# Performance work log

Measured on AMD Instinct MI355X. Metric: run time of the kernel, lower is better.

## Reference

```python
import jax, jax.numpy as jnp
import numpy as np

D_MODEL = 1024
NUM_HEADS = 16
HEAD_DIM = D_MODEL // NUM_HEADS
ROPE_THETA = 10000.0


def apply_rope(x):
    # x: (B, H, S, d_k) interleaved-pair RoPE, angles pos / theta^(2i/d_k)
    S, d_k = x.shape[-2], x.shape[-1]
    inv_freq = ROPE_THETA ** (jnp.arange(0, d_k, 2, dtype=jnp.float32) / d_k)
    ang = jnp.arange(S, dtype=jnp.float32)[:, None] / inv_freq[None, :]  # (S, d_k/2)
    cos, sin = jnp.cos(ang), jnp.sin(ang)
    xp = x.reshape(x.shape[:-1] + (d_k // 2, 2))
    x0, x1 = xp[..., 0], xp[..., 1]
    out = jnp.stack([x0 * cos - x1 * sin, x0 * sin + x1 * cos], axis=-1)
    return out.reshape(x.shape)


def setup_inputs() -> dict:
    key = jax.random.key(0)
    k1, k2, k3 = jax.random.split(key, 3)
    B, S = 2, 2048
    std = 2.0 / (D_MODEL + 3 * D_MODEL)
    std_o = 2.0 / (D_MODEL + D_MODEL)
    return {
        "x": jax.random.normal(k1, (B, S, D_MODEL), dtype=jnp.float32),
        "W_qkv": jax.random.normal(k2, (3 * D_MODEL, D_MODEL), dtype=jnp.float32) * std,
        "W_o": jax.random.normal(k3, (D_MODEL, D_MODEL), dtype=jnp.float32) * std_o,
    }


def reference(x, W_qkv, W_o):
    B, S, d_model = x.shape
    H, d_k = NUM_HEADS, HEAD_DIM
    qkv = jnp.einsum('bsi,oi->bso', x, W_qkv)  # (B, S, 3*d_model)
    Q, K, V = jnp.split(qkv, 3, axis=-1)
    # (B, S, d_model) -> (B, H, S, d_k)
    def to_heads(t):
        return t.reshape(B, S, H, d_k).transpose(0, 2, 1, 3)
    Q, K, V = to_heads(Q), to_heads(K), to_heads(V)
    Q, K = apply_rope(Q), apply_rope(K)
    scores = jnp.einsum('bhqd,bhkd->bhqk', Q, K) / jnp.sqrt(jnp.float32(d_k))
    causal = jnp.tril(jnp.ones((S, S), dtype=bool))
    scores = jnp.where(causal, scores, -jnp.inf)
    attn = jax.nn.softmax(scores, axis=-1)
    out = jnp.einsum('bhqk,bhkd->bhqd', attn, V)
    out = out.transpose(0, 2, 1, 3).reshape(B, S, d_model)
    return jnp.einsum('bsi,oi->bso', out, W_o)
```

## Files before the change

kernel.cpp:

```cpp
#include <hip/hip_runtime.h>
#include <math.h>

#define kB 2
#define kS 2048
#define kD 1024
#define kH 16
#define kDk 64
#define kM (kB * kS)
#define kLog2Theta 13.287712379549449
#define C_SCALE 0.18033688011112042f

typedef __attribute__((ext_vector_type(4))) float f32x4;
typedef __attribute__((ext_vector_type(16))) float f32x16;
typedef __attribute__((ext_vector_type(8))) __bf16 bf16x8;

__device__ __forceinline__ ushort f2bf(float f) {
  uint u = __float_as_uint(f);
  return (ushort)((u + 0x7fffu + ((u >> 16) & 1u)) >> 16);
}
__device__ __forceinline__ uint cvt_pk_bf16(float lo, float hi) {
  uint r;
  asm("v_cvt_pk_bf16_f32 %0, %1, %2" : "=v"(r) : "v"(lo), "v"(hi));
  return r;
}

typedef __attribute__((address_space(1))) void gvoid;
typedef __attribute__((address_space(3))) void lvoid;
__device__ __forceinline__ void load_lds16(const void* g, void* l) {
  __builtin_amdgcn_global_load_lds((gvoid*)g, (lvoid*)l, 16, 0, 0);
}

__global__ __launch_bounds__(256) void rope_table_kernel(float2* __restrict__ tab) {
  const int i = blockIdx.x * 256 + threadIdx.x;
  const int s = i >> 5, p = i & 31;
  const double ang = (double)s * exp2(-(double)p * (kLog2Theta / 32.0));
  tab[i] = make_float2((float)cos(ang), (float)sin(ang));
}

__global__ __launch_bounds__(256) void cast_all_kernel(
    const float* __restrict__ x, const float* __restrict__ wq,
    const float* __restrict__ wo, ushort* __restrict__ xb,
    ushort* __restrict__ wqb, ushort* __restrict__ wob) {
  const int i = blockIdx.x * 256 + threadIdx.x;
  const float* src;
  ushort* dst;
  int off;
  if (i < 1048576) {
    src = x; dst = xb; off = i;
  } else if (i < 1048576 + 786432) {
    src = wq; dst = wqb; off = i - 1048576;
  } else {
    src = wo; dst = wob; off = i - 1835008;
  }
  const float4 v = reinterpret_cast<const float4*>(src)[off];
  ushort4 o;
  o.x = f2bf(v.x); o.y = f2bf(v.y); o.z = f2bf(v.z); o.w = f2bf(v.w);
  reinterpret_cast<ushort4*>(dst)[off] = o;
}

__global__ __launch_bounds__(256) void vtrans_kernel(
    const ushort* __restrict__ v, ushort* __restrict__ vt) {
  __shared__ ushort T[64 * 66];
  const int bh = blockIdx.y, st = blockIdx.x;
  const int tid = threadIdx.x;
  const ushort* vp = v + ((size_t)bh * kS + st * 64) * kDk;
#pragma unroll
  for (int u = 0; u < 2; ++u) {
    const int idx = u * 256 + tid;
    const int r = idx >> 3, c = (idx & 7) << 3;
    const uint4 d4 = *reinterpret_cast<const uint4*>(&vp[r * 64 + c]);
    uint* dst = reinterpret_cast<uint*>(&T[r * 66 + c]);
    dst[0] = d4.x; dst[1] = d4.y; dst[2] = d4.z; dst[3] = d4.w;
  }
  __syncthreads();
  const int d = tid >> 2, seg = tid & 3;
  ushort tmp[16];
#pragma unroll
  for (int j = 0; j < 16; ++j) tmp[j] = T[(seg * 16 + j) * 66 + d];
  ushort* dst = vt + ((size_t)bh * kDk + d) * kS + st * 64 + seg * 16;
  *reinterpret_cast<uint4*>(dst) = *reinterpret_cast<uint4*>(tmp);
  *reinterpret_cast<uint4*>(dst + 8) = *reinterpret_cast<uint4*>(tmp + 8);
}

__device__ __forceinline__ void gemm_mainloop(
    const ushort* __restrict__ A, const ushort* __restrict__ B,
    int m0, int n0, int tid, ushort* As, ushort* Bs, f32x4 acc[4][4]) {
  const int lane = tid & 63;
  const int wid = tid >> 6;
  const int wm = (wid >> 1) << 6, wn = (wid & 1) << 6;
  const int fr = lane & 15, fq = lane >> 4;

  for (int k0 = 0; k0 < kD; k0 += 64) {
#pragma unroll
    for (int u = 0; u < 4; ++u) {
      const int c = u * 256 + tid;
      const int r = c >> 3, kc = (c & 7) << 3;
      load_lds16(&A[(size_t)(m0 + r) * kD + k0 + kc], &As[c << 3]);
      load_lds16(&B[(size_t)(n0 + r) * kD + k0 + kc], &Bs[c << 3]);
    }
    __syncthreads();
#pragma unroll
    for (int kk = 0; kk < 64; kk += 32) {
      bf16x8 af[4], bfr[4];
#pragma unroll
      for (int f = 0; f < 4; ++f) {
        af[f]  = *reinterpret_cast<const bf16x8*>(&As[(wm + f * 16 + fr) * 64 + kk + fq * 8]);
        bfr[f] = *reinterpret_cast<const bf16x8*>(&Bs[(wn + f * 16 + fr) * 64 + kk + fq * 8]);
      }
#pragma unroll
      for (int i = 0; i < 4; ++i)
#pragma unroll
        for (int j = 0; j < 4; ++j)
          acc[i][j] = __builtin_amdgcn_mfma_f32_16x16x32_bf16(af[i], bfr[j], acc[i][j], 0, 0, 0);
    }
    __syncthreads();
  }
}

__global__ __launch_bounds__(256) void qkv_mfma_kernel(
    const ushort* __restrict__ xb, const ushort* __restrict__ wqb,
    const float2* __restrict__ tab,
    ushort* __restrict__ q, ushort* __restrict__ k, ushort* __restrict__ v) {
  __shared__ ushort As[128 * 64];
  __shared__ ushort Bs[128 * 64];
  const int tid = threadIdx.x;
  const int m0 = blockIdx.y << 7, n0 = blockIdx.x << 7;
  f32x4 acc[4][4];
#pragma unroll
  for (int i = 0; i < 4; ++i)
#pragma unroll
    for (int j = 0; j < 4; ++j) acc[i][j] = {0.f, 0.f, 0.f, 0.f};

  gemm_mainloop(xb, wqb, m0, n0, tid, As, Bs, acc);

  const int lane = tid & 63;
  const int wid = tid >> 6;
  const int wm = (wid >> 1) << 6, wn = (wid & 1) << 6;
  const int fr = lane & 15, fq = lane >> 4;
  const int t = n0 >> 10;
  ushort* dst = (t == 0) ? q : (t == 1) ? k : v;

#pragma unroll
  for (int i = 0; i < 4; ++i) {
    const int mbase = m0 + wm + i * 16 + fq * 4;
#pragma unroll
    for (int j = 0; j < 4; ++j) {
      const int n = n0 + wn + j * 16 + fr;
      const int h = (n >> 6) & 15, d = n & 63;
#pragma unroll
      for (int r = 0; r < 4; ++r) {
        const int m = mbase + r;
        const int b = m >> 11, s = m & (kS - 1);
        float val = acc[i][j][r];
        if (t < 2) {
          const float2 cs = tab[(s << 5) + (d >> 1)];
          const float partner = __shfl_xor(val, 1);
          val = (d & 1) ? (partner * cs.y + val * cs.x)
                        : (val * cs.x - partner * cs.y);
        }
        if (t == 0) val *= C_SCALE;
        dst[(((size_t)((b << 4) + h) << 11) + s) * kDk + d] = f2bf(val);
      }
    }
  }
}

__global__ __launch_bounds__(256) void proj_mfma_kernel(
    const ushort* __restrict__ ab, const ushort* __restrict__ wob,
    float* __restrict__ out) {
  __shared__ ushort As[128 * 64];
  __shared__ ushort Bs[128 * 64];
  const int tid = threadIdx.x;
  const int m0 = blockIdx.y << 7, n0 = blockIdx.x << 7;
  f32x4 acc[4][4];
#pragma unroll
  for (int i = 0; i < 4; ++i)
#pragma unroll
    for (int j = 0; j < 4; ++j) acc[i][j] = {0.f, 0.f, 0.f, 0.f};

  gemm_mainloop(ab, wob, m0, n0, tid, As, Bs, acc);

  const int lane = tid & 63;
  const int wid = tid >> 6;
  const int wm = (wid >> 1) << 6, wn = (wid & 1) << 6;
  const int fr = lane & 15, fq = lane >> 4;
#pragma unroll
  for (int i = 0; i < 4; ++i)
#pragma unroll
    for (int j = 0; j < 4; ++j)
#pragma unroll
      for (int r = 0; r < 4; ++r)
        out[(size_t)(m0 + wm + i * 16 + fq * 4 + r) * kD + n0 + wn + j * 16 + fr] =
            acc[i][j][r];
}

__global__ __launch_bounds__(256) void attn_mfma_kernel(
    const ushort* __restrict__ q, const ushort* __restrict__ k,
    const ushort* __restrict__ vt, ushort* __restrict__ ob) {
  __shared__ ushort smem[32768];
  const int tid = threadIdx.x;
  const int lane = tid & 63;
  const int wq = tid >> 6;
  const int l5 = lane >> 5;
  const int ln = lane & 31;
  const int swz = (ln & 7) << 4;

  const int idx = blockIdx.x;
  const int grp = idx >> 5, bh = idx & 31;
  const int qi = (grp < 8) ? (15 - grp) : (grp - 8);
  const int qb = qi << 7;
  const int nt = qi + 1;

  const ushort* qp = q + (size_t)bh * kS * kDk;
  const ushort* kp = k + (size_t)bh * kS * kDk;
  const ushort* vp = vt + (size_t)bh * kDk * kS;

  bf16x8 bq[4];
#pragma unroll
  for (int kk = 0; kk < 4; ++kk)
    bq[kk] = *reinterpret_cast<const bf16x8*>(
        &qp[(size_t)(qb + wq * 32 + ln) * kDk + kk * 16 + l5 * 8]);

  f32x16 acc_o[2];
#pragma unroll
  for (int db = 0; db < 2; ++db)
#pragma unroll
    for (int r = 0; r < 16; ++r) acc_o[db][r] = 0.f;
  float l_run = 0.f;

  auto stage = [&](int kt, int buf) {
    ushort* Kd = smem + buf * 16384;
    ushort* Vd = Kd + 8192;
#pragma unroll
    for (int u = 0; u < 4; ++u) {
      const int c = u * 256 + tid;
      {
        const int r = c >> 3, sl = c & 7;
        load_lds16(&kp[(size_t)(kt * 128 + r) * kDk + ((sl ^ (r & 7)) << 3)],
                   &Kd[c << 3]);
      }
      {
        const int r = c >> 4, sl = c & 15;
        load_lds16(&vp[(size_t)r * kS + kt * 128 + ((sl ^ (r & 7)) << 3)],
                   &Vd[c << 3]);
      }
    }
  };

  stage(0, 0);

  for (int kt = 0; kt < nt; ++kt) {
    const int cur = kt & 1;
    __syncthreads();
    if (kt + 1 < nt) stage(kt + 1, cur ^ 1);

    const char* KsB = reinterpret_cast<const char*>(smem + cur * 16384);
    const char* VtsB = KsB + 16384;

    f32x16 accs[4];
    __builtin_amdgcn_s_setprio(1);
#pragma unroll
    for (int cb = 0; cb < 4; ++cb) {
#pragma unroll
      for (int r = 0; r < 16; ++r) accs[cb][r] = 0.f;
#pragma unroll
      for (int kk = 0; kk < 4; ++kk) {
        const bf16x8 av = *reinterpret_cast<const bf16x8*>(
            KsB + (cb * 32 + ln) * 128 + ((kk * 32 + l5 * 16) ^ swz));
        accs[cb] = __builtin_amdgcn_mfma_f32_32x32x16_bf16(av, bq[kk], accs[cb], 0, 0, 0);
      }
    }
    __builtin_amdgcn_s_setprio(0);

    if (kt == qi) {
      const int lim = (wq << 5) + ln;
#pragma unroll
      for (int cb = 0; cb < 4; ++cb)
#pragma unroll
        for (int r = 0; r < 16; ++r) {
          const int key = cb * 32 + (r & 3) + 8 * (r >> 2) + 4 * l5;
          if (key > lim) accs[cb][r] = -INFINITY;
        }
    }

    uint c8[4][8];
    float lsum = 0.f;
#pragma unroll
    for (int cb = 0; cb < 4; ++cb) {
      float s0 = 0.f, s1 = 0.f, s2 = 0.f, s3 = 0.f;
      float p[16];
#pragma unroll
      for (int r = 0; r < 16; ++r) {
        p[r] = exp2f(accs[cb][r]);
        if ((r & 3) == 0) s0 += p[r];
        else if ((r & 3) == 1) s1 += p[r];
        else if ((r & 3) == 2) s2 += p[r];
        else s3 += p[r];
      }
      lsum += (s0 + s1) + (s2 + s3);
#pragma unroll
      for (int t = 0; t < 8; ++t)
        c8[cb][t] = cvt_pk_bf16(p[2 * t], p[2 * t + 1]);
    }
    l_run += lsum;

    __builtin_amdgcn_s_setprio(1);
#pragma unroll
    for (int kb = 0; kb < 8; ++kb) {
      const int cb = kb >> 1, base = (kb & 1) * 4;
      const uint a0 = c8[cb][base + 0], a1 = c8[cb][base + 1];
      const uint b0 = c8[cb][base + 2], b1 = c8[cb][base + 3];
      const uint sa0 = (uint)__shfl_xor((int)a0, 32);
      const uint sa1 = (uint)__shfl_xor((int)a1, 32);
      const uint sb0 = (uint)__shfl_xor((int)b0, 32);
      const uint sb1 = (uint)__shfl_xor((int)b1, 32);
      uint4 dw;
      dw.x = l5 ? sb0 : a0;
      dw.y = l5 ? sb1 : a1;
      dw.z = l5 ? b0 : sa0;
      dw.w = l5 ? b1 : sa1;
      const bf16x8 pa = *reinterpret_cast<const bf16x8*>(&dw);
#pragma unroll
      for (int db = 0; db < 2; ++db) {
        const bf16x8 av = *reinterpret_cast<const bf16x8*>(
            VtsB + (db * 32 + ln) * 256 + ((kb * 32 + l5 * 16) ^ swz));
        acc_o[db] = __builtin_amdgcn_mfma_f32_32x32x16_bf16(av, pa, acc_o[db], 0, 0, 0);
      }
    }
    __builtin_amdgcn_s_setprio(0);
  }

  const float l_tot = l_run + __shfl_xor(l_run, 32);
  const float linv = 1.f / l_tot;

  __syncthreads();
  char* OsB = reinterpret_cast<char*>(smem);
  const int orow = wq * 32 + ln;
#pragma unroll
  for (int db = 0; db < 2; ++db)
#pragma unroll
    for (int t = 0; t < 8; ++t) {
      const int reg = 2 * t;
      const int d = db * 32 + (reg & 3) + 8 * (reg >> 2) + 4 * l5;
      const uint pk2 = cvt_pk_bf16(acc_o[db][reg] * linv, acc_o[db][reg + 1] * linv);
      *reinterpret_cast<uint*>(OsB + orow * 128 + ((d * 2) ^ swz)) = pk2;
    }
  __syncthreads();
  const int b = bh >> 4, h = bh & 15;
  const int qrw = tid >> 1, half = tid & 1;
  ushort* orow_g = ob + ((size_t)(b * kS + qb + qrw)) * kD + h * kDk + half * 32;
#pragma unroll
  for (int sl = 0; sl < 4; ++sl) {
    const uint4 vdat = *reinterpret_cast<const uint4*>(
        OsB + qrw * 128 + ((half * 64 + sl * 16) ^ ((qrw & 7) << 4)));
    *reinterpret_cast<uint4*>(orow_g + sl * 8) = vdat;
  }
}

extern "C" void kernel_launch(void* const* d_in, const int* in_sizes, int n_in,
                              void* d_out, int out_size, void* d_ws,
                              size_t ws_size, hipStream_t stream) {
  const float* x = (const float*)d_in[0];
  const float* wqkv = (const float*)d_in[1];
  const float* wo = (const float*)d_in[2];
  float* out = (float*)d_out;
  char* w = (char*)d_ws;
  const size_t MB = 1024 * 1024;
  ushort* qb  = (ushort*)(w + 0 * MB);
  ushort* kb  = (ushort*)(w + 8 * MB);
  ushort* vb  = (ushort*)(w + 16 * MB);
  ushort* xb  = (ushort*)(w + 24 * MB);
  ushort* wqb = (ushort*)(w + 32 * MB);
  ushort* wob = (ushort*)(w + 38 * MB);
  float2* tab = (float2*)(w + 40 * MB);
  ushort* vtb = (ushort*)(w + 41 * MB);
  ushort* attnb = xb;

  hipLaunchKernelGGL(rope_table_kernel, dim3(256), dim3(256), 0, stream, tab);
  hipLaunchKernelGGL(cast_all_kernel, dim3(8192), dim3(256), 0, stream,
                     x, wqkv, wo, xb, wqb, wob);
  hipLaunchKernelGGL(qkv_mfma_kernel, dim3(3 * kD / 128, kM / 128), dim3(256),
                     0, stream, xb, wqb, tab, qb, kb, vb);
  hipLaunchKernelGGL(vtrans_kernel, dim3(kS / 64, kB * kH), dim3(256), 0,
                     stream, vb, vtb);
  hipLaunchKernelGGL(attn_mfma_kernel, dim3(512), dim3(256), 0, stream,
                     qb, kb, vtb, attnb);
  hipLaunchKernelGGL(proj_mfma_kernel, dim3(kD / 128, kM / 128), dim3(256), 0,
                     stream, attnb, wob, out);
}
```

Before: 163.2 us.

## Use 256x256 double-buffered swizzled LDS GEMM tiles for QKV and output projections

```diff
diff --git a/kernel.cpp b/kernel.cpp
--- a/kernel.cpp
+++ b/kernel.cpp
@@ -7,6 +7,7 @@
 #define kH 16
 #define kDk 64
 #define kM (kB * kS)
+#define kNT (kD / 64)
 #define kLog2Theta 13.287712379549449
 #define C_SCALE 0.18033688011112042f
 
@@ -82,70 +83,107 @@
   *reinterpret_cast<uint4*>(dst + 8) = *reinterpret_cast<uint4*>(tmp + 8);
 }
 
-__device__ __forceinline__ void gemm_mainloop(
+__device__ __forceinline__ void gemm256_mainloop(
     const ushort* __restrict__ A, const ushort* __restrict__ B,
-    int m0, int n0, int tid, ushort* As, ushort* Bs, f32x4 acc[4][4]) {
+    int m0, int n0, int tid,
+    ushort* As0, ushort* Bs0, ushort* As1, ushort* Bs1,
+    f32x4 (&acc)[8][4]) {
   const int lane = tid & 63;
-  const int wid = tid >> 6;
-  const int wm = (wid >> 1) << 6, wn = (wid & 1) << 6;
+  const int wmi = (tid >> 6) >> 2;
+  const int wni = (tid >> 6) & 3;
   const int fr = lane & 15, fq = lane >> 4;
 
-  for (int k0 = 0; k0 < kD; k0 += 64) {
-#pragma unroll
-    for (int u = 0; u < 4; ++u) {
-      const int c = u * 256 + tid;
-      const int r = c >> 3, kc = (c & 7) << 3;
-      load_lds16(&A[(size_t)(m0 + r) * kD + k0 + kc], &As[c << 3]);
-      load_lds16(&B[(size_t)(n0 + r) * kD + k0 + kc], &Bs[c << 3]);
-    }
-    __syncthreads();
-#pragma unroll
-    for (int kk = 0; kk < 64; kk += 32) {
-      bf16x8 af[4], bfr[4];
-#pragma unroll
-      for (int f = 0; f < 4; ++f) {
-        af[f]  = *reinterpret_cast<const bf16x8*>(&As[(wm + f * 16 + fr) * 64 + kk + fq * 8]);
-        bfr[f] = *reinterpret_cast<const bf16x8*>(&Bs[(wn + f * 16 + fr) * 64 + kk + fq * 8]);
-      }
-#pragma unroll
-      for (int i = 0; i < 4; ++i)
-#pragma unroll
-        for (int j = 0; j < 4; ++j)
-          acc[i][j] = __builtin_amdgcn_mfma_f32_16x16x32_bf16(af[i], bfr[j], acc[i][j], 0, 0, 0);
-    }
-    __syncthreads();
-  }
-}
-
-__global__ __launch_bounds__(256) void qkv_mfma_kernel(
+  auto stage_tile = [&](int k0, ushort* Ad, ushort* Bd) {
+#pragma unroll
+    for (int half = 0; half < 2; ++half)
+#pragma unroll
+      for (int u = 0; u < 2; ++u) {
+        const int c = u * 512 + tid;
+        const int r = c >> 3, sl = c & 7;
+        const int gcol = k0 + ((sl ^ (r & 7)) << 3);
+        const int loff = ((half * 128 + r) << 6) + (sl << 3);
+        load_lds16(&A[(size_t)(m0 + half * 128 + r) * kD + gcol], &Ad[loff]);
+        load_lds16(&B[(size_t)(n0 + half * 128 + r) * kD + gcol], &Bd[loff]);
+      }
+  };
+  auto frag = [&](const ushort* S, int row, int kk) -> bf16x8 {
+    const int off = ((kk << 5) + (fq << 3)) ^ ((fr & 7) << 3);
+    return *reinterpret_cast<const bf16x8*>(&S[(row << 6) + off]);
+  };
+
+  stage_tile(0, As0, Bs0);
+  asm volatile("s_waitcnt vmcnt(0)" ::: "memory");
+  __builtin_amdgcn_s_barrier();
+
+  auto tile = [&](int kt, const ushort* cA, const ushort* cB,
+                  ushort* nA, ushort* nB) {
+#pragma unroll
+    for (int p = 0; p < 4; ++p) {
+      const int iset = (p & 1) << 2, jset = (p >> 1) << 1;
+      bf16x8 af[4][2], bfv[2][2];
+#pragma unroll
+      for (int i2 = 0; i2 < 4; ++i2)
+#pragma unroll
+        for (int kk = 0; kk < 2; ++kk)
+          af[i2][kk] = frag(cA, (wmi << 7) + (iset + i2) * 16 + fr, kk);
+#pragma unroll
+      for (int j2 = 0; j2 < 2; ++j2)
+#pragma unroll
+        for (int kk = 0; kk < 2; ++kk)
+          bfv[j2][kk] = frag(cB, (wni << 6) + (jset + j2) * 16 + fr, kk);
+      if (p == 0 && kt + 1 < kNT) stage_tile((kt + 1) << 6, nA, nB);
+      __builtin_amdgcn_s_barrier();
+      asm volatile("s_waitcnt lgkmcnt(0)" ::: "memory");
+      __builtin_amdgcn_sched_barrier(0);
+      __builtin_amdgcn_s_setprio(1);
+#pragma unroll
+      for (int i2 = 0; i2 < 4; ++i2)
+#pragma unroll
+        for (int j2 = 0; j2 < 2; ++j2)
+#pragma unroll
+          for (int kk = 0; kk < 2; ++kk)
+            acc[iset + i2][jset + j2] = __builtin_amdgcn_mfma_f32_16x16x32_bf16(
+                af[i2][kk], bfv[j2][kk], acc[iset + i2][jset + j2], 0, 0, 0);
+      __builtin_amdgcn_s_setprio(0);
+      if (p == 3) asm volatile("s_waitcnt vmcnt(0)" ::: "memory");
+      __builtin_amdgcn_s_barrier();
+    }
+  };
+
+  for (int kt = 0; kt < kNT; kt += 2) {
+    tile(kt, As0, Bs0, As1, Bs1);
+    tile(kt + 1, As1, Bs1, As0, Bs0);
+  }
+}
+
+__global__ __launch_bounds__(512, 2) void qkv_mfma_kernel(
     const ushort* __restrict__ xb, const ushort* __restrict__ wqb,
     const float2* __restrict__ tab,
     ushort* __restrict__ q, ushort* __restrict__ k, ushort* __restrict__ v) {
-  __shared__ ushort As[128 * 64];
-  __shared__ ushort Bs[128 * 64];
+  __shared__ ushort As0[256 * 64], Bs0[256 * 64];
+  __shared__ ushort As1[256 * 64], Bs1[256 * 64];
   const int tid = threadIdx.x;
-  const int m0 = blockIdx.y << 7, n0 = blockIdx.x << 7;
-  f32x4 acc[4][4];
-#pragma unroll
-  for (int i = 0; i < 4; ++i)
+  const int m0 = blockIdx.y << 8, n0 = blockIdx.x << 8;
+  f32x4 acc[8][4];
+#pragma unroll
+  for (int i = 0; i < 8; ++i)
 #pragma unroll
     for (int j = 0; j < 4; ++j) acc[i][j] = {0.f, 0.f, 0.f, 0.f};
 
-  gemm_mainloop(xb, wqb, m0, n0, tid, As, Bs, acc);
+  gemm256_mainloop(xb, wqb, m0, n0, tid, As0, Bs0, As1, Bs1, acc);
 
   const int lane = tid & 63;
-  const int wid = tid >> 6;
-  const int wm = (wid >> 1) << 6, wn = (wid & 1) << 6;
+  const int wmi = (tid >> 6) >> 2, wni = (tid >> 6) & 3;
   const int fr = lane & 15, fq = lane >> 4;
   const int t = n0 >> 10;
   ushort* dst = (t == 0) ? q : (t == 1) ? k : v;
 
 #pragma unroll
-  for (int i = 0; i < 4; ++i) {
-    const int mbase = m0 + wm + i * 16 + fq * 4;
+  for (int i = 0; i < 8; ++i) {
+    const int mbase = m0 + (wmi << 7) + i * 16 + fq * 4;
 #pragma unroll
     for (int j = 0; j < 4; ++j) {
-      const int n = n0 + wn + j * 16 + fr;
+      const int n = n0 + (wni << 6) + j * 16 + fr;
       const int h = (n >> 6) & 15, d = n & 63;
 #pragma unroll
       for (int r = 0; r < 4; ++r) {
@@ -165,33 +203,32 @@
   }
 }
 
-__global__ __launch_bounds__(256) void proj_mfma_kernel(
+__global__ __launch_bounds__(512, 2) void proj_mfma_kernel(
     const ushort* __restrict__ ab, const ushort* __restrict__ wob,
     float* __restrict__ out) {
-  __shared__ ushort As[128 * 64];
-  __shared__ ushort Bs[128 * 64];
+  __shared__ ushort As0[256 * 64], Bs0[256 * 64];
+  __shared__ ushort As1[256 * 64], Bs1[256 * 64];
   const int tid = threadIdx.x;
-  const int m0 = blockIdx.y << 7, n0 = blockIdx.x << 7;
-  f32x4 acc[4][4];
-#pragma unroll
-  for (int i = 0; i < 4; ++i)
+  const int m0 = blockIdx.y << 8, n0 = blockIdx.x << 8;
+  f32x4 acc[8][4];
+#pragma unroll
+  for (int i = 0; i < 8; ++i)
 #pragma unroll
     for (int j = 0; j < 4; ++j) acc[i][j] = {0.f, 0.f, 0.f, 0.f};
 
-  gemm_mainloop(ab, wob, m0, n0, tid, As, Bs, acc);
+  gemm256_mainloop(ab, wob, m0, n0, tid, As0, Bs0, As1, Bs1, acc);
 
   const int lane = tid & 63;
-  const int wid = tid >> 6;
-  const int wm = (wid >> 1) << 6, wn = (wid & 1) << 6;
+  const int wmi = (tid >> 6) >> 2, wni = (tid >> 6) & 3;
   const int fr = lane & 15, fq = lane >> 4;
 #pragma unroll
-  for (int i = 0; i < 4; ++i)
+  for (int i = 0; i < 8; ++i)
 #pragma unroll
     for (int j = 0; j < 4; ++j)
 #pragma unroll
       for (int r = 0; r < 4; ++r)
-        out[(size_t)(m0 + wm + i * 16 + fq * 4 + r) * kD + n0 + wn + j * 16 + fr] =
-            acc[i][j][r];
+        out[(size_t)(m0 + (wmi << 7) + i * 16 + fq * 4 + r) * kD +
+            n0 + (wni << 6) + j * 16 + fr] = acc[i][j][r];
 }
 
 __global__ __launch_bounds__(256) void attn_mfma_kernel(
@@ -379,12 +416,12 @@
   hipLaunchKernelGGL(rope_table_kernel, dim3(256), dim3(256), 0, stream, tab);
   hipLaunchKernelGGL(cast_all_kernel, dim3(8192), dim3(256), 0, stream,
                      x, wqkv, wo, xb, wqb, wob);
-  hipLaunchKernelGGL(qkv_mfma_kernel, dim3(3 * kD / 128, kM / 128), dim3(256),
+  hipLaunchKernelGGL(qkv_mfma_kernel, dim3(3 * kD / 256, kM / 256), dim3(512),
                      0, stream, xb, wqb, tab, qb, kb, vb);
   hipLaunchKernelGGL(vtrans_kernel, dim3(kS / 64, kB * kH), dim3(256), 0,
                      stream, vb, vtb);
   hipLaunchKernelGGL(attn_mfma_kernel, dim3(512), dim3(256), 0, stream,
                      qb, kb, vtb, attnb);
-  hipLaunchKernelGGL(proj_mfma_kernel, dim3(kD / 128, kM / 128), dim3(256), 0,
+  hipLaunchKernelGGL(proj_mfma_kernel, dim3(kD / 256, kM / 256), dim3(512), 0,
                      stream, attnb, wob, out);
 }
```

Result: slower. 176.8 us, median of 4 (+8.3%).

## Rewrite GEMM mainloop with double-buffered LDS, 32x32 MFMA and larger QKV tiles

Applied to the files above, without the earlier changes.

```diff
diff --git a/kernel.cpp b/kernel.cpp
--- a/kernel.cpp
+++ b/kernel.cpp
@@ -7,6 +7,7 @@
 #define kH 16
 #define kDk 64
 #define kM (kB * kS)
+#define kNT (kD / 64)
 #define kLog2Theta 13.287712379549449
 #define C_SCALE 0.18033688011112042f
 
@@ -82,74 +83,139 @@
   *reinterpret_cast<uint4*>(dst + 8) = *reinterpret_cast<uint4*>(tmp + 8);
 }
 
-__device__ __forceinline__ void gemm_mainloop(
+template <int BM, int BN, int WM, int WN>
+__device__ __forceinline__ void gemm_sub(
     const ushort* __restrict__ A, const ushort* __restrict__ B,
-    int m0, int n0, int tid, ushort* As, ushort* Bs, f32x4 acc[4][4]) {
+    int m0, int n0, int tid,
+    ushort* As0, ushort* Bs0, ushort* As1, ushort* Bs1,
+    f32x16 (&acc)[BM / (WM * 32)][BN / (WN * 32)]) {
+  constexpr int TM = BM / (WM * 32);
+  constexpr int TN = BN / (WN * 32);
+  constexpr int NTHR = WM * WN * 64;
+  constexpr int LGK = TM + TN;
   const int lane = tid & 63;
+  const int ln = lane & 31, l5 = lane >> 5;
   const int wid = tid >> 6;
-  const int wm = (wid >> 1) << 6, wn = (wid & 1) << 6;
-  const int fr = lane & 15, fq = lane >> 4;
-
-  for (int k0 = 0; k0 < kD; k0 += 64) {
-#pragma unroll
-    for (int u = 0; u < 4; ++u) {
-      const int c = u * 256 + tid;
-      const int r = c >> 3, kc = (c & 7) << 3;
-      load_lds16(&A[(size_t)(m0 + r) * kD + k0 + kc], &As[c << 3]);
-      load_lds16(&B[(size_t)(n0 + r) * kD + k0 + kc], &Bs[c << 3]);
-    }
+  const int wmi = wid / WN, wni = wid % WN;
+
+  auto stage_tile = [&](int k0, ushort* Ad, ushort* Bd) {
+#pragma unroll
+    for (int t = 0; t < BM * 8 / NTHR; ++t) {
+      const int c = t * NTHR + tid;
+      const int h = c & 1, r = (c >> 1) & 31, kk = (c >> 6) & 3, rb = c >> 8;
+      load_lds16(&A[(size_t)(m0 + rb * 32 + r) * kD + k0 + kk * 16 + h * 8],
+                 &Ad[c * 8]);
+    }
+#pragma unroll
+    for (int t = 0; t < BN * 8 / NTHR; ++t) {
+      const int c = t * NTHR + tid;
+      const int h = c & 1, r = (c >> 1) & 31, kk = (c >> 6) & 3, rb = c >> 8;
+      load_lds16(&B[(size_t)(n0 + rb * 32 + r) * kD + k0 + kk * 16 + h * 8],
+                 &Bd[c * 8]);
+    }
+  };
+  auto rd = [&](const ushort* S, int blk, int kk) -> bf16x8 {
+    return *reinterpret_cast<const bf16x8*>(
+        &S[((blk * 4 + kk) * 32 + ln) * 16 + l5 * 8]);
+  };
+
+  bf16x8 aX[TM], bX[TN], aY[TM], bY[TN];
+  auto rdX = [&](const ushort* cA, const ushort* cB, int kk) {
+#pragma unroll
+    for (int i = 0; i < TM; ++i) aX[i] = rd(cA, wmi * TM + i, kk);
+#pragma unroll
+    for (int j = 0; j < TN; ++j) bX[j] = rd(cB, wni * TN + j, kk);
+  };
+  auto rdY = [&](const ushort* cA, const ushort* cB, int kk) {
+#pragma unroll
+    for (int i = 0; i < TM; ++i) aY[i] = rd(cA, wmi * TM + i, kk);
+#pragma unroll
+    for (int j = 0; j < TN; ++j) bY[j] = rd(cB, wni * TN + j, kk);
+  };
+  auto mmaX = [&]() {
+    __builtin_amdgcn_s_setprio(1);
+#pragma unroll
+    for (int i = 0; i < TM; ++i)
+#pragma unroll
+      for (int j = 0; j < TN; ++j)
+        acc[i][j] = __builtin_amdgcn_mfma_f32_32x32x16_bf16(
+            aX[i], bX[j], acc[i][j], 0, 0, 0);
+    __builtin_amdgcn_s_setprio(0);
+  };
+  auto mmaY = [&]() {
+    __builtin_amdgcn_s_setprio(1);
+#pragma unroll
+    for (int i = 0; i < TM; ++i)
+#pragma unroll
+      for (int j = 0; j < TN; ++j)
+        acc[i][j] = __builtin_amdgcn_mfma_f32_32x32x16_bf16(
+            aY[i], bY[j], acc[i][j], 0, 0, 0);
+    __builtin_amdgcn_s_setprio(0);
+  };
+
+  stage_tile(0, As0, Bs0);
+  __syncthreads();
+
+  auto tile = [&](const ushort* cA, const ushort* cB, bool pf, int k0n,
+                  ushort* nA, ushort* nB) {
+    rdX(cA, cB, 0);
+    if (pf) stage_tile(k0n, nA, nB);
+    rdY(cA, cB, 1);
+    asm volatile("s_waitcnt lgkmcnt(%0)" ::"n"(LGK) : "memory");
+    __builtin_amdgcn_sched_barrier(0);
+    mmaX();
+    rdX(cA, cB, 2);
+    asm volatile("s_waitcnt lgkmcnt(%0)" ::"n"(LGK) : "memory");
+    __builtin_amdgcn_sched_barrier(0);
+    mmaY();
+    rdY(cA, cB, 3);
+    asm volatile("s_waitcnt lgkmcnt(%0)" ::"n"(LGK) : "memory");
+    __builtin_amdgcn_sched_barrier(0);
+    mmaX();
+    asm volatile("s_waitcnt lgkmcnt(0)" :: : "memory");
+    __builtin_amdgcn_sched_barrier(0);
+    mmaY();
     __syncthreads();
-#pragma unroll
-    for (int kk = 0; kk < 64; kk += 32) {
-      bf16x8 af[4], bfr[4];
-#pragma unroll
-      for (int f = 0; f < 4; ++f) {
-        af[f]  = *reinterpret_cast<const bf16x8*>(&As[(wm + f * 16 + fr) * 64 + kk + fq * 8]);
-        bfr[f] = *reinterpret_cast<const bf16x8*>(&Bs[(wn + f * 16 + fr) * 64 + kk + fq * 8]);
-      }
-#pragma unroll
-      for (int i = 0; i < 4; ++i)
-#pragma unroll
-        for (int j = 0; j < 4; ++j)
-          acc[i][j] = __builtin_amdgcn_mfma_f32_16x16x32_bf16(af[i], bfr[j], acc[i][j], 0, 0, 0);
-    }
-    __syncthreads();
+  };
+
+  for (int kt = 0; kt < kNT; kt += 2) {
+    tile(As0, Bs0, kt + 1 < kNT, (kt + 1) << 6, As1, Bs1);
+    tile(As1, Bs1, kt + 2 < kNT, (kt + 2) << 6, As0, Bs0);
   }
 }
 
-__global__ __launch_bounds__(256) void qkv_mfma_kernel(
+__global__ __launch_bounds__(512) void qkv_mfma_kernel(
     const ushort* __restrict__ xb, const ushort* __restrict__ wqb,
     const float2* __restrict__ tab,
     ushort* __restrict__ q, ushort* __restrict__ k, ushort* __restrict__ v) {
-  __shared__ ushort As[128 * 64];
-  __shared__ ushort Bs[128 * 64];
+  __shared__ ushort As0[256 * 64], Bs0[256 * 64];
+  __shared__ ushort As1[256 * 64], Bs1[256 * 64];
   const int tid = threadIdx.x;
-  const int m0 = blockIdx.y << 7, n0 = blockIdx.x << 7;
-  f32x4 acc[4][4];
+  const int m0 = blockIdx.y << 8, n0 = blockIdx.x << 8;
+  f32x16 acc[4][2];
 #pragma unroll
   for (int i = 0; i < 4; ++i)
 #pragma unroll
-    for (int j = 0; j < 4; ++j) acc[i][j] = {0.f, 0.f, 0.f, 0.f};
-
-  gemm_mainloop(xb, wqb, m0, n0, tid, As, Bs, acc);
-
-  const int lane = tid & 63;
-  const int wid = tid >> 6;
-  const int wm = (wid >> 1) << 6, wn = (wid & 1) << 6;
-  const int fr = lane & 15, fq = lane >> 4;
+    for (int j = 0; j < 2; ++j)
+#pragma unroll
+      for (int r = 0; r < 16; ++r) acc[i][j][r] = 0.f;
+
+  gemm_sub<256, 256, 2, 4>(xb, wqb, m0, n0, tid, As0, Bs0, As1, Bs1, acc);
+
+  const int lane = tid & 63, ln = lane & 31, l5 = lane >> 5;
+  const int wid = tid >> 6, wmi = wid >> 2, wni = wid & 3;
   const int t = n0 >> 10;
   ushort* dst = (t == 0) ? q : (t == 1) ? k : v;
 
 #pragma unroll
-  for (int i = 0; i < 4; ++i) {
-    const int mbase = m0 + wm + i * 16 + fq * 4;
-#pragma unroll
-    for (int j = 0; j < 4; ++j) {
-      const int n = n0 + wn + j * 16 + fr;
+  for (int i = 0; i < 4; ++i)
+#pragma unroll
+    for (int j = 0; j < 2; ++j) {
+      const int n = n0 + (wni * 2 + j) * 32 + ln;
       const int h = (n >> 6) & 15, d = n & 63;
 #pragma unroll
-      for (int r = 0; r < 4; ++r) {
-        const int m = mbase + r;
+      for (int r = 0; r < 16; ++r) {
+        const int m = m0 + (wmi * 4 + i) * 32 + (r & 3) + 8 * (r >> 2) + 4 * l5;
         const int b = m >> 11, s = m & (kS - 1);
         float val = acc[i][j][r];
         if (t < 2) {
@@ -162,36 +228,38 @@
         dst[(((size_t)((b << 4) + h) << 11) + s) * kDk + d] = f2bf(val);
       }
     }
-  }
 }
 
 __global__ __launch_bounds__(256) void proj_mfma_kernel(
     const ushort* __restrict__ ab, const ushort* __restrict__ wob,
     float* __restrict__ out) {
-  __shared__ ushort As[128 * 64];
-  __shared__ ushort Bs[128 * 64];
+  __shared__ ushort As0[128 * 64], Bs0[128 * 64];
+  __shared__ ushort As1[128 * 64], Bs1[128 * 64];
   const int tid = threadIdx.x;
   const int m0 = blockIdx.y << 7, n0 = blockIdx.x << 7;
-  f32x4 acc[4][4];
-#pragma unroll
-  for (int i = 0; i < 4; ++i)
-#pragma unroll
-    for (int j = 0; j < 4; ++j) acc[i][j] = {0.f, 0.f, 0.f, 0.f};
-
-  gemm_mainloop(ab, wob, m0, n0, tid, As, Bs, acc);
-
-  const int lane = tid & 63;
-  const int wid = tid >> 6;
-  const int wm = (wid >> 1) << 6, wn = (wid & 1) << 6;
-  const int fr = lane & 15, fq = lane >> 4;
-#pragma unroll
-  for (int i = 0; i < 4; ++i)
-#pragma unroll
-    for (int j = 0; j < 4; ++j)
-#pragma unroll
-      for (int r = 0; r < 4; ++r)
-        out[(size_t)(m0 + wm + i * 16 + fq * 4 + r) * kD + n0 + wn + j * 16 + fr] =
-            acc[i][j][r];
+  f32x16 acc[2][2];
+#pragma unroll
+  for (int i = 0; i < 2; ++i)
+#pragma unroll
+    for (int j = 0; j < 2; ++j)
+#pragma unroll
+      for (int r = 0; r < 16; ++r) acc[i][j][r] = 0.f;
+
+  gemm_sub<128, 128, 2, 2>(ab, wob, m0, n0, tid, As0, Bs0, As1, Bs1, acc);
+
+  const int lane = tid & 63, ln = lane & 31, l5 = lane >> 5;
+  const int wid = tid >> 6, wmi = wid >> 1, wni = wid & 1;
+#pragma unroll
+  for (int i = 0; i < 2; ++i)
+#pragma unroll
+    for (int j = 0; j < 2; ++j) {
+      const int n = n0 + (wni * 2 + j) * 32 + ln;
+#pragma unroll
+      for (int r = 0; r < 16; ++r) {
+        const int m = m0 + (wmi * 2 + i) * 32 + (r & 3) + 8 * (r >> 2) + 4 * l5;
+        out[(size_t)m * kD + n] = acc[i][j][r];
+      }
+    }
 }
 
 __global__ __launch_bounds__(256) void attn_mfma_kernel(
@@ -379,7 +447,7 @@
   hipLaunchKernelGGL(rope_table_kernel, dim3(256), dim3(256), 0, stream, tab);
   hipLaunchKernelGGL(cast_all_kernel, dim3(8192), dim3(256), 0, stream,
                      x, wqkv, wo, xb, wqb, wob);
-  hipLaunchKernelGGL(qkv_mfma_kernel, dim3(3 * kD / 128, kM / 128), dim3(256),
+  hipLaunchKernelGGL(qkv_mfma_kernel, dim3(3 * kD / 256, kM / 256), dim3(512),
                      0, stream, xb, wqb, tab, qb, kb, vb);
   hipLaunchKernelGGL(vtrans_kernel, dim3(kS / 64, kB * kH), dim3(256), 0,
                      stream, vb, vtb);
```

New measurement: 150.1 us. -8.0%, faster.

## Double-buffer GEMM mainloop with XOR-swizzled LDS and prefetch overlap

Applied to the files above, without the earlier changes.

```diff
diff --git a/kernel.cpp b/kernel.cpp
--- a/kernel.cpp
+++ b/kernel.cpp
@@ -7,6 +7,7 @@
 #define kH 16
 #define kDk 64
 #define kM (kB * kS)
+#define kNT (kD / 64)
 #define kLog2Theta 13.287712379549449
 #define C_SCALE 0.18033688011112042f
 
@@ -82,38 +83,64 @@
   *reinterpret_cast<uint4*>(dst + 8) = *reinterpret_cast<uint4*>(tmp + 8);
 }
 
-__device__ __forceinline__ void gemm_mainloop(
+__device__ __forceinline__ void gemm128_mainloop(
     const ushort* __restrict__ A, const ushort* __restrict__ B,
-    int m0, int n0, int tid, ushort* As, ushort* Bs, f32x4 acc[4][4]) {
+    int m0, int n0, int tid,
+    ushort* As0, ushort* Bs0, ushort* As1, ushort* Bs1,
+    f32x4 (&acc)[4][4]) {
   const int lane = tid & 63;
   const int wid = tid >> 6;
   const int wm = (wid >> 1) << 6, wn = (wid & 1) << 6;
   const int fr = lane & 15, fq = lane >> 4;
 
-  for (int k0 = 0; k0 < kD; k0 += 64) {
+  auto stage = [&](int k0, ushort* Ad, ushort* Bd) {
 #pragma unroll
     for (int u = 0; u < 4; ++u) {
       const int c = u * 256 + tid;
-      const int r = c >> 3, kc = (c & 7) << 3;
-      load_lds16(&A[(size_t)(m0 + r) * kD + k0 + kc], &As[c << 3]);
-      load_lds16(&B[(size_t)(n0 + r) * kD + k0 + kc], &Bs[c << 3]);
-    }
-    __syncthreads();
-#pragma unroll
-    for (int kk = 0; kk < 64; kk += 32) {
-      bf16x8 af[4], bfr[4];
+      const int r = c >> 3, sl = c & 7;
+      const int col = k0 + ((sl ^ (r & 7)) << 3);
+      load_lds16(&A[(size_t)(m0 + r) * kD + col], &Ad[c << 3]);
+      load_lds16(&B[(size_t)(n0 + r) * kD + col], &Bd[c << 3]);
+    }
+  };
+  auto rdfrag = [&](const ushort* S, int row, int kk) -> bf16x8 {
+    const int off = ((kk << 5) + (fq << 3)) ^ ((row & 7) << 3);
+    return *reinterpret_cast<const bf16x8*>(&S[(row << 6) + off]);
+  };
+
+  stage(0, As0, Bs0);
+
+  auto tile = [&](const ushort* cA, const ushort* cB, ushort* nA, ushort* nB,
+                  bool pf, int k0n) {
+    asm volatile("s_waitcnt vmcnt(0)" ::: "memory");
+    __builtin_amdgcn_s_barrier();
+    __builtin_amdgcn_sched_barrier(0);
+    bf16x8 af[2][4], bf_[2][4];
+#pragma unroll
+    for (int kk = 0; kk < 2; ++kk)
 #pragma unroll
       for (int f = 0; f < 4; ++f) {
-        af[f]  = *reinterpret_cast<const bf16x8*>(&As[(wm + f * 16 + fr) * 64 + kk + fq * 8]);
-        bfr[f] = *reinterpret_cast<const bf16x8*>(&Bs[(wn + f * 16 + fr) * 64 + kk + fq * 8]);
-      }
+        af[kk][f]  = rdfrag(cA, wm + f * 16 + fr, kk);
+        bf_[kk][f] = rdfrag(cB, wn + f * 16 + fr, kk);
+      }
+    if (pf) stage(k0n, nA, nB);
+    asm volatile("s_waitcnt lgkmcnt(0)" ::: "memory");
+    __builtin_amdgcn_sched_barrier(0);
+    __builtin_amdgcn_s_setprio(1);
+#pragma unroll
+    for (int kk = 0; kk < 2; ++kk)
 #pragma unroll
       for (int i = 0; i < 4; ++i)
 #pragma unroll
         for (int j = 0; j < 4; ++j)
-          acc[i][j] = __builtin_amdgcn_mfma_f32_16x16x32_bf16(af[i], bfr[j], acc[i][j], 0, 0, 0);
-    }
-    __syncthreads();
+          acc[i][j] = __builtin_amdgcn_mfma_f32_16x16x32_bf16(
+              af[kk][i], bf_[kk][j], acc[i][j], 0, 0, 0);
+    __builtin_amdgcn_s_setprio(0);
+  };
+
+  for (int t = 0; t < kNT; t += 2) {
+    tile(As0, Bs0, As1, Bs1, true, (t + 1) << 6);
+    tile(As1, Bs1, As0, Bs0, t + 2 < kNT, (t + 2) << 6);
   }
 }
 
@@ -121,8 +148,8 @@
     const ushort* __restrict__ xb, const ushort* __restrict__ wqb,
     const float2* __restrict__ tab,
     ushort* __restrict__ q, ushort* __restrict__ k, ushort* __restrict__ v) {
-  __shared__ ushort As[128 * 64];
-  __shared__ ushort Bs[128 * 64];
+  __shared__ ushort As0[128 * 64], Bs0[128 * 64];
+  __shared__ ushort As1[128 * 64], Bs1[128 * 64];
   const int tid = threadIdx.x;
   const int m0 = blockIdx.y << 7, n0 = blockIdx.x << 7;
   f32x4 acc[4][4];
@@ -131,7 +158,7 @@
 #pragma unroll
     for (int j = 0; j < 4; ++j) acc[i][j] = {0.f, 0.f, 0.f, 0.f};
 
-  gemm_mainloop(xb, wqb, m0, n0, tid, As, Bs, acc);
+  gemm128_mainloop(xb, wqb, m0, n0, tid, As0, Bs0, As1, Bs1, acc);
 
   const int lane = tid & 63;
   const int wid = tid >> 6;
@@ -168,8 +195,8 @@
 __global__ __launch_bounds__(256) void proj_mfma_kernel(
     const ushort* __restrict__ ab, const ushort* __restrict__ wob,
     float* __restrict__ out) {
-  __shared__ ushort As[128 * 64];
-  __shared__ ushort Bs[128 * 64];
+  __shared__ ushort As0[128 * 64], Bs0[128 * 64];
+  __shared__ ushort As1[128 * 64], Bs1[128 * 64];
   const int tid = threadIdx.x;
   const int m0 = blockIdx.y << 7, n0 = blockIdx.x << 7;
   f32x4 acc[4][4];
@@ -178,7 +205,7 @@
 #pragma unroll
     for (int j = 0; j < 4; ++j) acc[i][j] = {0.f, 0.f, 0.f, 0.f};
 
-  gemm_mainloop(ab, wob, m0, n0, tid, As, Bs, acc);
+  gemm128_mainloop(ab, wob, m0, n0, tid, As0, Bs0, As1, Bs1, acc);
 
   const int lane = tid & 63;
   const int wid = tid >> 6;
```

Measured after the change: 149.2 us. -8.6%, faster.
